# Performance work log

Hardware: AMD Instinct MI355X
Metric: run time of the kernel (lower is better)

Reference implementation:

```python
import jax, jax.numpy as jnp
import numpy as np

B, C, D = 16384, 4096, 512
ALPHA = 0.1
BETA = 0.25


def setup_inputs() -> dict:
    key = jax.random.key(0)
    kx, kc = jax.random.split(key)
    x = jax.random.normal(kx, (B, D), dtype=jnp.float32)
    codes = jax.random.normal(kc, (1, C, D), dtype=jnp.float32)
    return {"x": x, "codes": codes}


def reference(x, codes):
    # x: (B, D), codes: (1, C, D). Eval-mode forward of Quantizer (l2 metric).
    d = x.shape[1]
    c = codes[0]                                  # (C, D)
    # squared l2 distance via expansion (same math as sum((x-c)^2, -1))
    x_sq = jnp.sum(x * x, axis=-1, keepdims=True)  # (B, 1)
    c_sq = jnp.sum(c * c, axis=-1)                 # (C,)
    dots = jnp.einsum('bd,cd->bc', x, c)           # (B, C)
    raw_distances = x_sq + c_sq[None, :] - 2.0 * dots
    distances = raw_distances / d / ALPHA          # scaling preserved for faithfulness
    indices = jnp.argmin(distances, axis=-1)       # (B,)
    quantized = c[indices]                         # (B, D) gather
    # commit loss: dist(x, stop_grad(quantized)); codebook loss: dist(stop_grad(x), quantized)
    diff_commit = x - jax.lax.stop_gradient(quantized)
    loss_commit = jnp.mean(jnp.sum(diff_commit * diff_commit, axis=-1))
    diff_code = jax.lax.stop_gradient(x) - quantized
    loss_codebook = jnp.mean(jnp.sum(diff_code * diff_code, axis=-1))
    loss = loss_commit + BETA * loss_codebook
    return quantized, indices, loss
```

## Files before the change

### kernel.cpp

```cpp
#include <hip/hip_runtime.h>

#define B_SZ 16384
#define C_SZ 4096
#define D_SZ 512

#define EPS 1.0f
#define DBIAS 1024.0f

typedef __attribute__((ext_vector_type(8))) short short8;
typedef __attribute__((ext_vector_type(4))) float floatx4;

__device__ inline unsigned short f2bf(float f) {
    unsigned u = __float_as_uint(f);
    unsigned r = u + 0x7FFFu + ((u >> 16) & 1u);
    return (unsigned short)(r >> 16);
}
__device__ inline void gload16(const void* g, void* l) {
    __builtin_amdgcn_global_load_lds(
        (const __attribute__((address_space(1))) void*)g,
        (__attribute__((address_space(3))) void*)l, 16, 0, 0);
}

__global__ __launch_bounds__(256) void convert_kernel(const float* __restrict__ x,
                                                      const float* __restrict__ codes,
                                                      unsigned short* __restrict__ xhi,
                                                      unsigned short* __restrict__ chi,
                                                      float* __restrict__ csq) {
    const int XB = (B_SZ * D_SZ) / 4 / 256;
    if (blockIdx.x < XB) {
        const int tid = blockIdx.x * 256 + threadIdx.x;
        const float4 v = ((const float4*)x)[tid];
        ((ushort4*)xhi)[tid] = make_ushort4(f2bf(v.x), f2bf(v.y), f2bf(v.z), f2bf(v.w));
    } else {
        const int t = threadIdx.x;
        const int wave = t >> 6;
        const int lane = t & 63;
        const int code = (blockIdx.x - XB) * 4 + wave;
        const float4* cp = (const float4*)(codes + (size_t)code * D_SZ);
        float s = 0.0f;
        #pragma unroll
        for (int u = 0; u < 2; ++u) {
            const float4 v = cp[lane + 64 * u];
            ((ushort4*)chi)[(size_t)code * (D_SZ / 4) + lane + 64 * u] =
                make_ushort4(f2bf(v.x), f2bf(v.y), f2bf(v.z), f2bf(v.w));
            s = fmaf(v.x, v.x, s); s = fmaf(v.y, v.y, s);
            s = fmaf(v.z, v.z, s); s = fmaf(v.w, v.w, s);
        }
        #pragma unroll
        for (int off = 32; off; off >>= 1) s += __shfl_down(s, off, 64);
        if (lane == 0) csq[code] = s;
    }
}

__global__ __launch_bounds__(512, 4) void gemm_argmin_kernel(
        const unsigned short* __restrict__ xhi,
        const unsigned short* __restrict__ chi,
        const float* __restrict__ csq,
        uint2* __restrict__ table) {
    __shared__ unsigned short sA[128][64];
    __shared__ unsigned short sB[128][64];

    const int t = threadIdx.x;
    const int wave = t >> 6;
    const int lane = t & 63;
    const int quad = lane >> 4;
    const int l15 = lane & 15;

    const int rowbase = blockIdx.y * 128;
    const int colbase = blockIdx.x * 128;
    const int wr = (wave >> 1) * 32;
    const int wc = (wave & 1) * 64;

    const unsigned short* gsrc;
    unsigned short(*ltile)[64];
    int rowoff;
    if (wave < 4) { gsrc = xhi + (size_t)rowbase * D_SZ; ltile = sA; rowoff = wave * 32; }
    else          { gsrc = chi + (size_t)colbase * D_SZ; ltile = sB; rowoff = (wave - 4) * 32; }
    const int lrow = lane >> 3;
    const int lchunk = (lane & 7) ^ (lrow & 7);
    const unsigned short* gbase = gsrc + (size_t)(rowoff + lrow) * D_SZ + lchunk * 8;

    float cs2[4];
    #pragma unroll
    for (int j = 0; j < 4; ++j)
        cs2[j] = fmaf(0.5f, csq[colbase + wc + j * 16 + l15], DBIAS);

    floatx4 acc[2][4];
    #pragma unroll
    for (int i = 0; i < 2; ++i)
        #pragma unroll
        for (int j = 0; j < 4; ++j) acc[i][j] = (floatx4)0.0f;

    for (int kt = 0; kt < D_SZ / 64; ++kt) {
        const unsigned short* g = gbase + kt * 64;
        #pragma unroll
        for (int inst = 0; inst < 4; ++inst)
            gload16(g + (size_t)(inst * 8) * D_SZ, &ltile[rowoff + inst * 8][0]);
        __syncthreads();

        #pragma unroll
        for (int ksub = 0; ksub < 2; ++ksub) {
            const int cc = ((ksub * 4 + quad) ^ (l15 & 7)) * 8;
            short8 a[2], b[4];
            #pragma unroll
            for (int i = 0; i < 2; ++i)
                a[i] = *(const short8*)&sA[wr + i * 16 + l15][cc];
            #pragma unroll
            for (int j = 0; j < 4; ++j)
                b[j] = *(const short8*)&sB[wc + j * 16 + l15][cc];
            #pragma unroll
            for (int i = 0; i < 2; ++i)
                #pragma unroll
                for (int j = 0; j < 4; ++j)
                    acc[i][j] = __builtin_amdgcn_mfma_f32_16x16x32_bf16(a[i], b[j], acc[i][j], 0, 0, 0);
        }
        __syncthreads();
    }

    const int hb = blockIdx.x * 2 + (wave & 1);

    #pragma unroll
    for (int i = 0; i < 2; ++i) {
        #pragma unroll
        for (int r = 0; r < 4; ++r) {
            unsigned k[4];
            #pragma unroll
            for (int j = 0; j < 4; ++j) {
                const float d = cs2[j] - acc[i][j][r];
                k[j] = (__float_as_uint(d) & 0xFFFFFFC0u) | (unsigned)(j * 16 + l15);
            }
            const unsigned lo1 = min(k[0], k[1]), hi1 = max(k[0], k[1]);
            const unsigned lo2 = min(k[2], k[3]), hi2 = max(k[2], k[3]);
            unsigned k1 = min(lo1, lo2);
            unsigned k2 = min(max(lo1, lo2), min(hi1, hi2));
            #pragma unroll
            for (int off = 8; off; off >>= 1) {
                const unsigned ok1 = (unsigned)__shfl_down((int)k1, off, 16);
                const unsigned ok2 = (unsigned)__shfl_down((int)k2, off, 16);
                const unsigned hi = max(k1, ok1);
                const unsigned w2 = (k1 < ok1) ? k2 : ok2;
                k1 = min(k1, ok1);
                k2 = min(hi, w2);
            }
            if (l15 == 0) {
                const int grow = rowbase + wr + i * 16 + quad * 4 + r;
                table[(size_t)grow * 64 + hb] = make_uint2(k1, k2);
            }
        }
    }
}

__global__ __launch_bounds__(256) void rerank_gather_loss_kernel(
        const float* __restrict__ x,
        const float* __restrict__ codes,
        const float* __restrict__ csq,
        const uint2* __restrict__ table,
        float* __restrict__ outq,
        float* __restrict__ out_idx_f,
        float* __restrict__ partials) {
    __shared__ float red[4];
    const int t = threadIdx.x;
    const int wave = t >> 6;
    const int lane = t & 63;
    const int row = blockIdx.x * 4 + wave;

    const uint2 e = table[(size_t)row * 64 + lane];
    const unsigned k1 = e.x, k2 = e.y;

    unsigned mk = k1;
    #pragma unroll
    for (int off = 32; off; off >>= 1)
        mk = min(mk, (unsigned)__shfl_xor((int)mk, off, 64));

    const float thr = __uint_as_float(mk & 0xFFFFFFC0u) + EPS;
    const float v1 = __uint_as_float(k1 & 0xFFFFFFC0u);
    const float v2 = __uint_as_float(k2 & 0xFFFFFFC0u);
    const unsigned long long b1 = __ballot(v1 <= thr);
    const unsigned long long b2 = __ballot(v2 <= thr);

    const unsigned long long bm = __ballot(k1 == mk);
    const int mhb = __ffsll(bm) - 1;
    int fin = mhb * 64 + (int)(mk & 63u);

    const float4* xp = (const float4*)(x + (size_t)row * D_SZ);
    const float4 x0 = xp[lane];
    const float4 x1 = xp[lane + 64];

    if (__popcll(b1) + __popcll(b2) > 1) {
        const int c1 = lane * 64 + (int)(k1 & 63u);
        const int c2 = lane * 64 + (int)(k2 & 63u);
        float bv = 3.4e38f; int bi = 0x7FFFFFFF;
        #pragma unroll
        for (int pass = 0; pass < 2; ++pass) {
            unsigned long long bb = pass ? b2 : b1;
            const int myc = pass ? c2 : c1;
            while (bb) {
                const int src = __ffsll((unsigned long long)bb) - 1;
                bb &= bb - 1;
                const int ci = __shfl(myc, src, 64);
                const float4* cp = (const float4*)(codes + (size_t)ci * D_SZ);
                const float4 c0 = cp[lane];
                const float4 c1v = cp[lane + 64];
                float s = 0.0f;
                s = fmaf(x0.x, c0.x, s); s = fmaf(x0.y, c0.y, s);
                s = fmaf(x0.z, c0.z, s); s = fmaf(x0.w, c0.w, s);
                s = fmaf(x1.x, c1v.x, s); s = fmaf(x1.y, c1v.y, s);
                s = fmaf(x1.z, c1v.z, s); s = fmaf(x1.w, c1v.w, s);
                #pragma unroll
                for (int off = 32; off; off >>= 1) s += __shfl_xor(s, off, 64);
                const float d = fmaf(0.5f, csq[ci], -s);
                if (d < bv || (d == bv && ci < bi)) { bv = d; bi = ci; }
            }
        }
        fin = bi;
    }

    const float4* qp = (const float4*)(codes + (size_t)fin * D_SZ);
    float4* op = (float4*)(outq + (size_t)row * D_SZ);
    const float4 q0 = qp[lane];
    const float4 q1 = qp[lane + 64];
    op[lane] = q0;
    op[lane + 64] = q1;
    float s = 0.0f;
    {
        const float d0 = x0.x - q0.x, d1 = x0.y - q0.y, d2 = x0.z - q0.z, d3 = x0.w - q0.w;
        const float d4 = x1.x - q1.x, d5 = x1.y - q1.y, d6 = x1.z - q1.z, d7 = x1.w - q1.w;
        s = d0 * d0 + d1 * d1 + d2 * d2 + d3 * d3 + d4 * d4 + d5 * d5 + d6 * d6 + d7 * d7;
    }
    #pragma unroll
    for (int off = 32; off; off >>= 1) s += __shfl_down(s, off, 64);
    if (lane == 0) {
        red[wave] = s;
        out_idx_f[row] = (float)fin;
    }
    __syncthreads();
    if (t == 0) partials[blockIdx.x] = red[0] + red[1] + red[2] + red[3];
}

__global__ __launch_bounds__(256) void loss_reduce_kernel(const float* __restrict__ partials,
                                                          float* __restrict__ loss_slot) {
    __shared__ float red[4];
    const int t = threadIdx.x;
    const int wave = t >> 6;
    const int lane = t & 63;
    float s = 0.0f;
    #pragma unroll
    for (int i = 0; i < (B_SZ / 4) / 256; ++i) s += partials[i * 256 + t];
    #pragma unroll
    for (int off = 32; off; off >>= 1) s += __shfl_down(s, off, 64);
    if (lane == 0) red[wave] = s;
    __syncthreads();
    if (t == 0)
        *loss_slot = (red[0] + red[1] + red[2] + red[3]) * (1.25f / (float)B_SZ);
}

extern "C" void kernel_launch(void* const* d_in, const int* in_sizes, int n_in,
                              void* d_out, int out_size, void* d_ws, size_t ws_size,
                              hipStream_t stream) {
    const float* x = (const float*)d_in[0];
    const float* codes = (const float*)d_in[1];

    float* outq = (float*)d_out;
    float* out_idx_f = outq + (size_t)B_SZ * D_SZ;
    float* loss_slot = out_idx_f + B_SZ;

    unsigned short* xhi = (unsigned short*)d_ws;
    unsigned short* chi = xhi + (size_t)B_SZ * D_SZ;
    float* csq = (float*)(chi + (size_t)C_SZ * D_SZ);
    uint2* table = (uint2*)(csq + C_SZ);
    float* partials = (float*)(table + (size_t)B_SZ * 64);

    const int XB = (B_SZ * D_SZ) / 4 / 256;
    const int CB = C_SZ / 4;
    convert_kernel<<<XB + CB, 256, 0, stream>>>(x, codes, xhi, chi, csq);
    gemm_argmin_kernel<<<dim3(C_SZ / 128, B_SZ / 128), 512, 0, stream>>>(xhi, chi, csq, table);
    rerank_gather_loss_kernel<<<B_SZ / 4, 256, 0, stream>>>(x, codes, csq, table, outq, out_idx_f, partials);
    loss_reduce_kernel<<<1, 256, 0, stream>>>(partials, loss_slot);
}
```

Before: 193.0 us.

## Fold final loss reduction into rerank kernel via last-block atomic counter; raise GEMM occupancy hint

```diff
diff --git a/kernel.cpp b/kernel.cpp
--- a/kernel.cpp
+++ b/kernel.cpp
@@ -25,8 +25,10 @@
                                                       const float* __restrict__ codes,
                                                       unsigned short* __restrict__ xhi,
                                                       unsigned short* __restrict__ chi,
-                                                      float* __restrict__ csq) {
+                                                      float* __restrict__ csq,
+                                                      unsigned* __restrict__ counter) {
     const int XB = (B_SZ * D_SZ) / 4 / 256;
+    if (blockIdx.x == 0 && threadIdx.x == 0) *counter = 0u;
     if (blockIdx.x < XB) {
         const int tid = blockIdx.x * 256 + threadIdx.x;
         const float4 v = ((const float4*)x)[tid];
@@ -52,7 +54,7 @@
     }
 }
 
-__global__ __launch_bounds__(512, 4) void gemm_argmin_kernel(
+__global__ __launch_bounds__(512, 6) void gemm_argmin_kernel(
         const unsigned short* __restrict__ xhi,
         const unsigned short* __restrict__ chi,
         const float* __restrict__ csq,
@@ -157,7 +159,9 @@
         const uint2* __restrict__ table,
         float* __restrict__ outq,
         float* __restrict__ out_idx_f,
-        float* __restrict__ partials) {
+        float* __restrict__ partials,
+        unsigned* __restrict__ counter,
+        float* __restrict__ loss_slot) {
     __shared__ float red[4];
     const int t = threadIdx.x;
     const int wave = t >> 6;
@@ -234,24 +238,27 @@
         out_idx_f[row] = (float)fin;
     }
     __syncthreads();
-    if (t == 0) partials[blockIdx.x] = red[0] + red[1] + red[2] + red[3];
-}
-
-__global__ __launch_bounds__(256) void loss_reduce_kernel(const float* __restrict__ partials,
-                                                          float* __restrict__ loss_slot) {
-    __shared__ float red[4];
-    const int t = threadIdx.x;
-    const int wave = t >> 6;
-    const int lane = t & 63;
-    float s = 0.0f;
-    #pragma unroll
-    for (int i = 0; i < (B_SZ / 4) / 256; ++i) s += partials[i * 256 + t];
-    #pragma unroll
-    for (int off = 32; off; off >>= 1) s += __shfl_down(s, off, 64);
-    if (lane == 0) red[wave] = s;
+
+    __shared__ bool amlast;
+    if (t == 0) {
+        partials[blockIdx.x] = red[0] + red[1] + red[2] + red[3];
+        __threadfence();
+        const unsigned old = atomicAdd(counter, 1u);
+        amlast = (old == (unsigned)(B_SZ / 4 - 1));
+    }
     __syncthreads();
-    if (t == 0)
-        *loss_slot = (red[0] + red[1] + red[2] + red[3]) * (1.25f / (float)B_SZ);
+    if (amlast) {
+        __threadfence();
+        float ls = 0.0f;
+        #pragma unroll
+        for (int i = 0; i < (B_SZ / 4) / 256; ++i) ls += partials[i * 256 + t];
+        #pragma unroll
+        for (int off = 32; off; off >>= 1) ls += __shfl_down(ls, off, 64);
+        if (lane == 0) red[wave] = ls;
+        __syncthreads();
+        if (t == 0)
+            *loss_slot = (red[0] + red[1] + red[2] + red[3]) * (1.25f / (float)B_SZ);
+    }
 }
 
 extern "C" void kernel_launch(void* const* d_in, const int* in_sizes, int n_in,
@@ -269,11 +276,12 @@
     float* csq = (float*)(chi + (size_t)C_SZ * D_SZ);
     uint2* table = (uint2*)(csq + C_SZ);
     float* partials = (float*)(table + (size_t)B_SZ * 64);
+    unsigned* counter = (unsigned*)(partials + B_SZ / 4);
 
     const int XB = (B_SZ * D_SZ) / 4 / 256;
     const int CB = C_SZ / 4;
-    convert_kernel<<<XB + CB, 256, 0, stream>>>(x, codes, xhi, chi, csq);
+    convert_kernel<<<XB + CB, 256, 0, stream>>>(x, codes, xhi, chi, csq, counter);
     gemm_argmin_kernel<<<dim3(C_SZ / 128, B_SZ / 128), 512, 0, stream>>>(xhi, chi, csq, table);
-    rerank_gather_loss_kernel<<<B_SZ / 4, 256, 0, stream>>>(x, codes, csq, table, outq, out_idx_f, partials);
-    loss_reduce_kernel<<<1, 256, 0, stream>>>(partials, loss_slot);
-}
+    rerank_gather_loss_kernel<<<B_SZ / 4, 256, 0, stream>>>(x, codes, csq, table, outq, out_idx_f,
+                                                            partials, counter, loss_slot);
+}
```

After: 317.7 us. +64.6%, slower.
